# Performance work log

Hardware: AMD Instinct MI355X
Metric: run time of the kernel (lower is better)

The kernel has to match this reference:

```python
import jax, jax.numpy as jnp
import numpy as np

D = 1024; H = 16; DH = 64; L = 24; S = 4096; DFF = 4096
QB = 7; NC = 2 ** QB; TOPK = 10; EOS = NC + 1
SCALE = float(1.0 / np.sqrt(DH))


def _ln(x, g):
    m = jnp.mean(x, axis=-1, keepdims=True)
    v = jnp.var(x, axis=-1, keepdims=True)
    return (x - m) * jax.lax.rsqrt(v + 1e-5) * g


def _mlp(h, w1, b1, w2, b2, w3, b3):
    h = jax.nn.relu(h @ w1 + b1)
    h = jax.nn.relu(h @ w2 + b2)
    return h @ w3 + b3


def _decode(x, k_cache, v_cache, ln1_g, Wq, Wk, Wv, Wo, ln2_g, Wg, Wu, Wd, lnf_g):
    # single-token decode through L pre-norm layers with KV cache
    def step(h, xs):
        l1, wq, wk, wv, wo, l2, wg, wu, wd, K, V = xs
        hn = _ln(h, l1)
        q = (hn @ wq).reshape(H, DH)
        kn = (hn @ wk).reshape(1, H, DH)
        vn = (hn @ wv).reshape(1, H, DH)
        Kf = jnp.concatenate([K, kn], axis=0)  # [S+1,H,DH]
        Vf = jnp.concatenate([V, vn], axis=0)
        att = jax.nn.softmax(jnp.einsum('hd,shd->hs', q, Kf) * SCALE, axis=-1)
        o = jnp.einsum('hs,shd->hd', att, Vf).reshape(D)
        h = h + o @ wo
        hn = _ln(h, l2)
        h = h + (jax.nn.gelu(hn @ wg) * (hn @ wu)) @ wd  # GLU FF
        return h, None

    res, _ = jax.lax.scan(step, x, (ln1_g, Wq, Wk, Wv, Wo, ln2_g, Wg, Wu, Wd, k_cache, v_cache))
    return _ln(res, lnf_g)


def setup_inputs() -> dict:
    key = jax.random.key(0)
    ks = jax.random.split(key, 40)
    def r(i, shape, s=0.02):
        return jax.random.normal(ks[i], shape, dtype=jnp.float32) * s
    inp = {
        'x': r(0, (D,), 1.0),
        'k_cache': r(1, (L, S, H, DH), 1.0),
        'v_cache': r(2, (L, S, H, DH), 1.0),
        'ln1_g': jnp.ones((L, D), jnp.float32),
        'Wq': r(3, (L, D, D)), 'Wk': r(4, (L, D, D)), 'Wv': r(5, (L, D, D)), 'Wo': r(6, (L, D, D)),
        'ln2_g': jnp.ones((L, D), jnp.float32),
        'Wg': r(7, (L, D, DFF)), 'Wu': r(8, (L, D, DFF)), 'Wd': r(9, (L, DFF, D)),
        'lnf_g': jnp.ones((D,), jnp.float32),
        'h1_w1': r(10, (D, D)), 'h1_b1': jnp.zeros((D,), jnp.float32),
        'h1_w2': r(11, (D, D)), 'h1_b2': jnp.zeros((D,), jnp.float32),
        'h1_w3': r(12, (D, NC + 2)), 'h1_b3': jnp.zeros((NC + 2,), jnp.float32),
        'h2_w1': r(13, (2 * D, D)), 'h2_b1': jnp.zeros((D,), jnp.float32),
        'h2_w2': r(14, (D, D)), 'h2_b2': jnp.zeros((D,), jnp.float32),
        'h2_w3': r(15, (D, NC)), 'h2_b3': jnp.zeros((NC,), jnp.float32),
        'h3_w1': r(16, (3 * D, D)), 'h3_b1': jnp.zeros((D,), jnp.float32),
        'h3_w2': r(17, (D, D)), 'h3_b2': jnp.zeros((D,), jnp.float32),
        'h3_w3': r(18, (D, NC)), 'h3_b3': jnp.zeros((NC,), jnp.float32),
        'c1_emb': r(19, (NC, D), 1.0),
        'c2_emb': r(20, (NC, D), 1.0),
    }
    return inp


def reference(x, k_cache, v_cache, ln1_g, Wq, Wk, Wv, Wo, ln2_g, Wg, Wu, Wd, lnf_g,
              h1_w1, h1_b1, h1_w2, h1_b2, h1_w3, h1_b3,
              h2_w1, h2_b1, h2_w2, h2_b2, h2_w3, h2_b3,
              h3_w1, h3_b1, h3_w2, h3_b2, h3_w3, h3_b3,
              c1_emb, c2_emb):
    res = _decode(x, k_cache, v_cache, ln1_g, Wq, Wk, Wv, Wo, ln2_g, Wg, Wu, Wd, lnf_g)

    k1, k2, k3 = jax.random.split(jax.random.key(42), 3)

    # stage 1: z coordinate (quantized) with EOS-masked top-k sampling
    logits_z = _mlp(res, h1_w1, h1_b1, h1_w2, h1_b2, h1_w3, h1_b3)  # [NC+2]
    tpz, tiz = jax.lax.top_k(jax.nn.softmax(logits_z), TOPK)
    is_eos = tiz[0] == EOS
    mp = tpz * (tiz != EOS).astype(tpz.dtype)
    mp = mp / mp.sum()
    z = jnp.where(is_eos, EOS, tiz[jax.random.categorical(k1, jnp.log(mp + 1e-9))])
    emb_z = c1_emb[jnp.minimum(z, NC - 1)]

    # stage 2: y coordinate
    logits_y = _mlp(jnp.concatenate([res, emb_z]), h2_w1, h2_b1, h2_w2, h2_b2, h2_w3, h2_b3)
    tpy, tiy = jax.lax.top_k(jax.nn.softmax(logits_y), TOPK)
    y = tiy[jax.random.categorical(k2, jnp.log(tpy + 1e-9))]
    emb_y = c2_emb[y]

    # stage 3: x coordinate
    logits_x = _mlp(jnp.concatenate([res, emb_z, emb_y]), h3_w1, h3_b1, h3_w2, h3_b2, h3_w3, h3_b3)
    tpx, tix = jax.lax.top_k(jax.nn.softmax(logits_x), TOPK)
    xc = tix[jax.random.categorical(k3, jnp.log(tpx + 1e-9))]

    xyz = jnp.stack([xc, y, z])
    logits_cat = jnp.concatenate([logits_z, logits_y, logits_x])  # [130+128+128]=386
    return xyz, logits_cat
```

## Files before the change

kernel.cpp:

```cpp
#include <hip/hip_runtime.h>
#include <cstdint>
#include <cstring>
#include <cmath>

constexpr int kH    = 16;
constexpr int kL    = 24;
constexpr int kS    = 4096;
constexpr int kEOS  = 129;
constexpr float kSCALE = 0.125f;
constexpr int kNS   = 32;
constexpr int kTOK  = kS / kNS;

struct G10 { float g[10]; };


__device__ __forceinline__ float wave_sum(float v) {
  v += __shfl_xor(v, 32, 64); v += __shfl_xor(v, 16, 64);
  v += __shfl_xor(v, 8, 64);  v += __shfl_xor(v, 4, 64);
  v += __shfl_xor(v, 2, 64);  v += __shfl_xor(v, 1, 64);
  return v;
}
__device__ __forceinline__ float wave_max(float v) {
  v = fmaxf(v, __shfl_xor(v, 32, 64)); v = fmaxf(v, __shfl_xor(v, 16, 64));
  v = fmaxf(v, __shfl_xor(v, 8, 64));  v = fmaxf(v, __shfl_xor(v, 4, 64));
  v = fmaxf(v, __shfl_xor(v, 2, 64));  v = fmaxf(v, __shfl_xor(v, 1, 64));
  return v;
}
__device__ __forceinline__ float block_sum4(float v, float* red) {
  v = wave_sum(v);
  if ((threadIdx.x & 63) == 0) red[threadIdx.x >> 6] = v;
  __syncthreads();
  float s = red[0] + red[1] + red[2] + red[3];
  __syncthreads();
  return s;
}
__device__ __forceinline__ float block_max4(float v, float* red) {
  v = wave_max(v);
  if ((threadIdx.x & 63) == 0) red[threadIdx.x >> 6] = v;
  __syncthreads();
  float s = fmaxf(fmaxf(red[0], red[1]), fmaxf(red[2], red[3]));
  __syncthreads();
  return s;
}

__device__ __forceinline__ void ln_stats(const float* __restrict__ h, float* red,
                                         float& mean, float& rs) {
  int tid = threadIdx.x;
  float v0 = h[tid], v1 = h[tid + 256], v2 = h[tid + 512], v3 = h[tid + 768];
  float s = block_sum4(v0 + v1 + v2 + v3, red);
  mean = s * (1.0f / 1024.0f);
  float d0 = v0 - mean, d1 = v1 - mean, d2 = v2 - mean, d3 = v3 - mean;
  float sq = block_sum4(d0 * d0 + d1 * d1 + d2 * d2 + d3 * d3, red);
  rs = 1.0f / sqrtf(sq * (1.0f / 1024.0f) + 1e-5f);
}

__device__ __forceinline__ float gelu_f(float x) {
  float t = tanhf(0.7978845608028654f * (x + 0.044715f * x * x * x));
  return 0.5f * x * (1.0f + t);
}


__global__ __launch_bounds__(256) void k_ln_qkv(const float* __restrict__ h,
                                                const float* __restrict__ g,
                                                const float* __restrict__ Wq,
                                                const float* __restrict__ Wk,
                                                const float* __restrict__ Wv,
                                                float* __restrict__ qkv_part,
                                                float* __restrict__ hres) {
  __shared__ float red4[4];
  __shared__ float xs[64];
  __shared__ float4 sh4[256];
  int tid = threadIdx.x;
  float mean, rs;
  ln_stats(h, red4, mean, rs);
  int by = blockIdx.y, rb = by * 64;
  if (tid < 64) xs[tid] = (h[rb + tid] - mean) * rs * g[rb + tid];
  if (blockIdx.x == 0 && tid < 64) hres[rb + tid] = h[rb + tid];
  __syncthreads();
  int c4 = tid & 63, w = tid >> 6;
  int vcol4 = blockIdx.x * 64 + c4;
  int mat = vcol4 >> 8;
  const float* W = (mat == 0) ? Wq : ((mat == 1) ? Wk : Wv);
  const float4* W4 = reinterpret_cast<const float4*>(W);
  int wcol4 = vcol4 & 255;
  float4 acc = {0.f, 0.f, 0.f, 0.f};
  int r0 = w * 16;
  #pragma unroll
  for (int i = 0; i < 16; ++i) {
    int j = r0 + i;
    float xv = xs[j];
    float4 wv = W4[(size_t)(rb + j) * 256 + wcol4];
    acc.x += xv * wv.x; acc.y += xv * wv.y; acc.z += xv * wv.z; acc.w += xv * wv.w;
  }
  sh4[tid] = acc;
  __syncthreads();
  if (tid < 64) {
    float4 a = sh4[tid], b = sh4[tid + 64], c = sh4[tid + 128], d = sh4[tid + 192];
    a.x += b.x + c.x + d.x; a.y += b.y + c.y + d.y;
    a.z += b.z + c.z + d.z; a.w += b.w + c.w + d.w;
    reinterpret_cast<float4*>(qkv_part)[(size_t)by * 768 + blockIdx.x * 64 + tid] = a;
  }
}

__global__ __launch_bounds__(256) void k_attn(const float* __restrict__ qkv_part,
                                              const float* __restrict__ Kc,
                                              const float* __restrict__ Vc,
                                              float* __restrict__ part) {
  __shared__ float4 q4[16];
  __shared__ float4 kn4[16];
  __shared__ float4 vn4[16];
  __shared__ float sc[132];
  __shared__ float red4[4];
  __shared__ float4 ored[16][17];
  int split = blockIdx.x, head = blockIdx.y;
  int tid = threadIdx.x;
  if (tid < 64) {
    float s = 0.f;
    #pragma unroll
    for (int p = 0; p < 16; ++p) s += qkv_part[p * 3072 + head * 64 + tid];
    ((float*)q4)[tid] = s;
  } else if (tid < 128) {
    int d = tid - 64; float s = 0.f;
    #pragma unroll
    for (int p = 0; p < 16; ++p) s += qkv_part[p * 3072 + 1024 + head * 64 + d];
    ((float*)kn4)[d] = s;
  } else if (tid < 192) {
    int d = tid - 128; float s = 0.f;
    #pragma unroll
    for (int p = 0; p < 16; ++p) s += qkv_part[p * 3072 + 2048 + head * 64 + d];
    ((float*)vn4)[d] = s;
  }
  __syncthreads();
  int base = split * kTOK;
  int count = kTOK + (split == kNS - 1 ? 1 : 0);
  int wv = tid >> 6, lane = tid & 63, grp = lane >> 4, l16 = lane & 15;
  float4 qf = q4[l16];
  for (int t = wv * 4 + grp; t < count; t += 16) {
    float4 kf = (t < kTOK)
      ? reinterpret_cast<const float4*>(Kc + (size_t)(base + t) * 1024 + head * 64)[l16]
      : kn4[l16];
    float d = qf.x * kf.x + qf.y * kf.y + qf.z * kf.z + qf.w * kf.w;
    d += __shfl_xor(d, 1, 16); d += __shfl_xor(d, 2, 16);
    d += __shfl_xor(d, 4, 16); d += __shfl_xor(d, 8, 16);
    if (l16 == 0) sc[t] = d * kSCALE;
  }
  __syncthreads();
  float v = (tid < count) ? sc[tid] : -1e30f;
  float m = block_max4(v, red4);
  float pexp = 0.f;
  if (tid < count) { pexp = expf(sc[tid] - m); sc[tid] = pexp; }
  float l = block_sum4(pexp, red4);
  float4 acc = {0.f, 0.f, 0.f, 0.f};
  for (int t = wv * 4 + grp; t < count; t += 16) {
    float4 vf = (t < kTOK)
      ? reinterpret_cast<const float4*>(Vc + (size_t)(base + t) * 1024 + head * 64)[l16]
      : vn4[l16];
    float p = sc[t];
    acc.x += p * vf.x; acc.y += p * vf.y; acc.z += p * vf.z; acc.w += p * vf.w;
  }
  ored[wv * 4 + grp][l16] = acc;
  __syncthreads();
  float* pp = &part[(size_t)(head * kNS + split) * 68];
  if (tid < 16) {
    float4 s = ored[0][tid];
    #pragma unroll
    for (int k = 1; k < 16; ++k) {
      float4 b = ored[k][tid];
      s.x += b.x; s.y += b.y; s.z += b.z; s.w += b.w;
    }
    reinterpret_cast<float4*>(pp + 4)[tid] = s;
  }
  if (tid == 0) { pp[0] = m; pp[1] = l; }
}

__global__ __launch_bounds__(256) void k_comb_wo(const float* __restrict__ part,
                                                 const float* __restrict__ Wo,
                                                 float* __restrict__ hout) {
  __shared__ float o[64];
  __shared__ float4 sh4[256];
  int tid = threadIdx.x;
  int head = blockIdx.y;
  if (tid < 64) {
    const float* pp = part + (size_t)(head * kNS) * 68;
    float m = -1e30f;
    for (int s = 0; s < kNS; ++s) m = fmaxf(m, pp[s * 68]);
    float l = 0.f, acc = 0.f;
    for (int s = 0; s < kNS; ++s) {
      float e = expf(pp[s * 68] - m);
      l += e * pp[s * 68 + 1];
      acc += e * pp[s * 68 + 4 + tid];
    }
    o[tid] = acc / l;
  }
  __syncthreads();
  int c4 = tid & 63, w = tid >> 6;
  int vcol4 = blockIdx.x * 64 + c4;
  const float4* W4 = reinterpret_cast<const float4*>(Wo);
  float4 acc = {0.f, 0.f, 0.f, 0.f};
  int r0 = w * 16;
  #pragma unroll
  for (int i = 0; i < 16; ++i) {
    int r = r0 + i;
    float xv = o[r];
    float4 wv = W4[(size_t)(head * 64 + r) * 256 + vcol4];
    acc.x += xv * wv.x; acc.y += xv * wv.y; acc.z += xv * wv.z; acc.w += xv * wv.w;
  }
  sh4[tid] = acc;
  __syncthreads();
  if (tid < 64) {
    float4 a = sh4[tid], b = sh4[tid + 64], c = sh4[tid + 128], d = sh4[tid + 192];
    a.x += b.x + c.x + d.x; a.y += b.y + c.y + d.y;
    a.z += b.z + c.z + d.z; a.w += b.w + c.w + d.w;
    int vcol = (blockIdx.x * 64 + tid) * 4;
    atomicAdd(&hout[vcol],     a.x);
    atomicAdd(&hout[vcol + 1], a.y);
    atomicAdd(&hout[vcol + 2], a.z);
    atomicAdd(&hout[vcol + 3], a.w);
  }
}

__global__ __launch_bounds__(256) void k_ln_gu(const float* __restrict__ h,
                                               const float* __restrict__ g,
                                               const float* __restrict__ Wg,
                                               const float* __restrict__ Wu,
                                               float* __restrict__ gu_part,
                                               float* __restrict__ hres) {
  __shared__ float red4[4];
  __shared__ float xs[64];
  __shared__ float4 sh4[256];
  int tid = threadIdx.x;
  float mean, rs;
  ln_stats(h, red4, mean, rs);
  int by = blockIdx.y, rb = by * 64;
  if (tid < 64) xs[tid] = (h[rb + tid] - mean) * rs * g[rb + tid];
  if (blockIdx.x == 0 && tid < 64) hres[rb + tid] = h[rb + tid];
  __syncthreads();
  int c4 = tid & 63, w = tid >> 6;
  int vcol4 = blockIdx.x * 64 + c4;
  int mat = vcol4 >> 10;
  const float4* W4 = reinterpret_cast<const float4*>(mat ? Wu : Wg);
  int wcol4 = vcol4 & 1023;
  float4 acc = {0.f, 0.f, 0.f, 0.f};
  int r0 = w * 16;
  #pragma unroll
  for (int i = 0; i < 16; ++i) {
    int j = r0 + i;
    float xv = xs[j];
    float4 wv = W4[(size_t)(rb + j) * 1024 + wcol4];
    acc.x += xv * wv.x; acc.y += xv * wv.y; acc.z += xv * wv.z; acc.w += xv * wv.w;
  }
  sh4[tid] = acc;
  __syncthreads();
  if (tid < 64) {
    float4 a = sh4[tid], b = sh4[tid + 64], c = sh4[tid + 128], d = sh4[tid + 192];
    a.x += b.x + c.x + d.x; a.y += b.y + c.y + d.y;
    a.z += b.z + c.z + d.z; a.w += b.w + c.w + d.w;
    reinterpret_cast<float4*>(gu_part)[(size_t)by * 2048 + blockIdx.x * 64 + tid] = a;
  }
}

__global__ __launch_bounds__(256) void k_act_wd(const float* __restrict__ gu_part,
                                                const float* __restrict__ Wd,
                                                float* __restrict__ hout) {
  __shared__ float xs[64];
  __shared__ float4 sh4[256];
  int tid = threadIdx.x;
  int by = blockIdx.y, rb = by * 64;
  if (tid < 64) {
    float gs = 0.f, us = 0.f;
    #pragma unroll
    for (int p = 0; p < 16; ++p) {
      gs += gu_part[p * 8192 + rb + tid];
      us += gu_part[p * 8192 + 4096 + rb + tid];
    }
    xs[tid] = gelu_f(gs) * us;
  }
  __syncthreads();
  int c4 = tid & 63, w = tid >> 6;
  int vcol4 = blockIdx.x * 64 + c4;
  const float4* W4 = reinterpret_cast<const float4*>(Wd);
  float4 acc = {0.f, 0.f, 0.f, 0.f};
  int r0 = w * 16;
  #pragma unroll
  for (int i = 0; i < 16; ++i) {
    int j = r0 + i;
    float xv = xs[j];
    float4 wv = W4[(size_t)(rb + j) * 256 + vcol4];
    acc.x += xv * wv.x; acc.y += xv * wv.y; acc.z += xv * wv.z; acc.w += xv * wv.w;
  }
  sh4[tid] = acc;
  __syncthreads();
  if (tid < 64) {
    float4 a = sh4[tid], b = sh4[tid + 64], c = sh4[tid + 128], d = sh4[tid + 192];
    a.x += b.x + c.x + d.x; a.y += b.y + c.y + d.y;
    a.z += b.z + c.z + d.z; a.w += b.w + c.w + d.w;
    int vcol = (blockIdx.x * 64 + tid) * 4;
    atomicAdd(&hout[vcol],     a.x);
    atomicAdd(&hout[vcol + 1], a.y);
    atomicAdd(&hout[vcol + 2], a.z);
    atomicAdd(&hout[vcol + 3], a.w);
  }
}


__global__ __launch_bounds__(256) void k_lnf(const float* __restrict__ h,
                                             const float* __restrict__ g,
                                             float* __restrict__ outv) {
  __shared__ float red4[4];
  int tid = threadIdx.x;
  float mean, rs;
  ln_stats(h, red4, mean, rs);
  #pragma unroll
  for (int k = 0; k < 4; ++k) {
    int i = tid + 256 * k;
    outv[i] = (h[i] - mean) * rs * g[i];
  }
}

__global__ __launch_bounds__(256) void k_head_g1(const float* __restrict__ x,
                                                 const float* __restrict__ W,
                                                 float* __restrict__ t1_part,
                                                 const float* __restrict__ b3,
                                                 float* __restrict__ logits, int n3) {
  __shared__ float4 sh4[256];
  int tid = threadIdx.x;
  int by = blockIdx.y, rb = by * 64;
  if (blockIdx.x == 0 && by == 0 && tid < n3) logits[tid] = b3[tid];
  int c4 = tid & 63, w = tid >> 6;
  int vcol4 = blockIdx.x * 64 + c4;
  const float4* W4 = reinterpret_cast<const float4*>(W);
  float4 acc = {0.f, 0.f, 0.f, 0.f};
  int r0 = w * 16;
  #pragma unroll
  for (int i = 0; i < 16; ++i) {
    int r = rb + r0 + i;
    float xv = x[r];
    float4 wv = W4[(size_t)r * 256 + vcol4];
    acc.x += xv * wv.x; acc.y += xv * wv.y; acc.z += xv * wv.z; acc.w += xv * wv.w;
  }
  sh4[tid] = acc;
  __syncthreads();
  if (tid < 64) {
    float4 a = sh4[tid], b = sh4[tid + 64], c = sh4[tid + 128], d = sh4[tid + 192];
    a.x += b.x + c.x + d.x; a.y += b.y + c.y + d.y;
    a.z += b.z + c.z + d.z; a.w += b.w + c.w + d.w;
    reinterpret_cast<float4*>(t1_part)[(size_t)by * 256 + blockIdx.x * 64 + tid] = a;
  }
}

__global__ __launch_bounds__(256) void k_head_g2(const float* __restrict__ t1_part,
                                                 int ny,
                                                 const float* __restrict__ b1,
                                                 const float* __restrict__ W,
                                                 float* __restrict__ t2_part) {
  __shared__ float xs[64];
  __shared__ float4 sh4[256];
  int tid = threadIdx.x;
  int by = blockIdx.y, rb = by * 64;
  if (tid < 64) {
    float s = b1[rb + tid];
    for (int p = 0; p < ny; ++p) s += t1_part[p * 1024 + rb + tid];
    xs[tid] = fmaxf(s, 0.f);
  }
  __syncthreads();
  int c4 = tid & 63, w = tid >> 6;
  int vcol4 = blockIdx.x * 64 + c4;
  const float4* W4 = reinterpret_cast<const float4*>(W);
  float4 acc = {0.f, 0.f, 0.f, 0.f};
  int r0 = w * 16;
  #pragma unroll
  for (int i = 0; i < 16; ++i) {
    int j = r0 + i;
    float xv = xs[j];
    float4 wv = W4[(size_t)(rb + j) * 256 + vcol4];
    acc.x += xv * wv.x; acc.y += xv * wv.y; acc.z += xv * wv.z; acc.w += xv * wv.w;
  }
  sh4[tid] = acc;
  __syncthreads();
  if (tid < 64) {
    float4 a = sh4[tid], b = sh4[tid + 64], c = sh4[tid + 128], d = sh4[tid + 192];
    a.x += b.x + c.x + d.x; a.y += b.y + c.y + d.y;
    a.z += b.z + c.z + d.z; a.w += b.w + c.w + d.w;
    reinterpret_cast<float4*>(t2_part)[(size_t)by * 256 + blockIdx.x * 64 + tid] = a;
  }
}

__global__ __launch_bounds__(256) void k_head_g3(const float* __restrict__ t2_part,
                                                 const float* __restrict__ b2,
                                                 const float* __restrict__ W,
                                                 float* __restrict__ logits, int n3) {
  __shared__ float xs[64];
  int tid = threadIdx.x;
  int rb = blockIdx.x * 64;
  if (tid < 64) {
    float s = b2[rb + tid];
    #pragma unroll
    for (int p = 0; p < 16; ++p) s += t2_part[p * 1024 + rb + tid];
    xs[tid] = fmaxf(s, 0.f);
  }
  __syncthreads();
  if (tid < n3) {
    float acc = 0.f;
    for (int i = 0; i < 64; ++i) acc += xs[i] * W[(size_t)(rb + i) * n3 + tid];
    atomicAdd(&logits[tid], acc);
  }
}


__global__ void k_sample1(const float* __restrict__ logits,
                          const float* __restrict__ c1_emb,
                          float* __restrict__ embdst,
                          float* __restrict__ out_xyz,
                          G10 gb) {
  __shared__ int zsh;
  int tid = threadIdx.x;
  if (tid == 0) {
    float p[130];
    float mx = -1e30f;
    for (int i = 0; i < 130; ++i) mx = fmaxf(mx, logits[i]);
    float s = 0.f;
    for (int i = 0; i < 130; ++i) { p[i] = expf(logits[i] - mx); s += p[i]; }
    for (int i = 0; i < 130; ++i) p[i] /= s;
    float tp[10]; int ti[10];
    for (int k = 0; k < 10; ++k) {
      float best = -1.f; int bi = 0;
      for (int i = 0; i < 130; ++i)
        if (p[i] > best) { best = p[i]; bi = i; }
      tp[k] = best; ti[k] = bi; p[bi] = -2.f;
    }
    int is_eos = (ti[0] == kEOS);
    float mp[10]; float ssum = 0.f;
    for (int k = 0; k < 10; ++k) {
      mp[k] = tp[k] * ((ti[k] != kEOS) ? 1.f : 0.f);
      ssum += mp[k];
    }
    float bestsc = -1e30f; int ba = 0;
    for (int k = 0; k < 10; ++k) {
      float sc = logf(mp[k] / ssum + 1e-9f) + gb.g[k];
      if (sc > bestsc) { bestsc = sc; ba = k; }
    }
    int z = is_eos ? kEOS : ti[ba];
    zsh = z;
    out_xyz[2] = (float)z;
  }
  __syncthreads();
  int zi = zsh; if (zi > 127) zi = 127;
  for (int i = tid; i < 1024; i += blockDim.x)
    embdst[i] = c1_emb[(size_t)zi * 1024 + i];
}

__global__ void k_sample23(const float* __restrict__ logits,
                           const float* __restrict__ emb,
                           float* __restrict__ embdst,
                           float* __restrict__ outslot,
                           G10 gb) {
  __shared__ int ysh;
  int tid = threadIdx.x;
  if (tid == 0) {
    float p[128];
    float mx = -1e30f;
    for (int i = 0; i < 128; ++i) mx = fmaxf(mx, logits[i]);
    float s = 0.f;
    for (int i = 0; i < 128; ++i) { p[i] = expf(logits[i] - mx); s += p[i]; }
    for (int i = 0; i < 128; ++i) p[i] /= s;
    float tp[10]; int ti[10];
    for (int k = 0; k < 10; ++k) {
      float best = -1.f; int bi = 0;
      for (int i = 0; i < 128; ++i)
        if (p[i] > best) { best = p[i]; bi = i; }
      tp[k] = best; ti[k] = bi; p[bi] = -2.f;
    }
    float bestsc = -1e30f; int ba = 0;
    for (int k = 0; k < 10; ++k) {
      float sc = logf(tp[k] + 1e-9f) + gb.g[k];
      if (sc > bestsc) { bestsc = sc; ba = k; }
    }
    int y = ti[ba];
    ysh = y;
    *outslot = (float)y;
  }
  __syncthreads();
  if (emb != nullptr) {
    int y = ysh;
    for (int i = tid; i < 1024; i += blockDim.x)
      embdst[i] = emb[(size_t)y * 1024 + i];
  }
}


static inline uint32_t rotl32(uint32_t x, uint32_t r) { return (x << r) | (x >> (32 - r)); }

static void threefry2x32(uint32_t k0, uint32_t k1, uint32_t x0, uint32_t x1,
                         uint32_t* o0, uint32_t* o1) {
  uint32_t ks0 = k0, ks1 = k1, ks2 = k0 ^ k1 ^ 0x1BD11BDAu;
  const uint32_t R0[4] = {13, 15, 26, 6};
  const uint32_t R1[4] = {17, 29, 16, 24};
  x0 += ks0; x1 += ks1;
  for (int j = 0; j < 4; ++j) { x0 += x1; x1 = rotl32(x1, R0[j]); x1 ^= x0; }
  x0 += ks1; x1 += ks2 + 1u;
  for (int j = 0; j < 4; ++j) { x0 += x1; x1 = rotl32(x1, R1[j]); x1 ^= x0; }
  x0 += ks2; x1 += ks0 + 2u;
  for (int j = 0; j < 4; ++j) { x0 += x1; x1 = rotl32(x1, R0[j]); x1 ^= x0; }
  x0 += ks0; x1 += ks1 + 3u;
  for (int j = 0; j < 4; ++j) { x0 += x1; x1 = rotl32(x1, R1[j]); x1 ^= x0; }
  x0 += ks1; x1 += ks2 + 4u;
  for (int j = 0; j < 4; ++j) { x0 += x1; x1 = rotl32(x1, R0[j]); x1 ^= x0; }
  x0 += ks2; x1 += ks0 + 5u;
  *o0 = x0; *o1 = x1;
}

static void gumbel10_part(uint32_t k0, uint32_t k1, float* g) {
  const float tiny = 1.1754943508222875e-38f;
  for (int i = 0; i < 10; ++i) {
    uint32_t a, c;
    threefry2x32(k0, k1, 0u, (uint32_t)i, &a, &c);
    uint32_t bits = a ^ c;
    uint32_t fb = (bits >> 9) | 0x3f800000u;
    float f; memcpy(&f, &fb, 4);
    f -= 1.0f;
    float u = f * (1.0f - tiny) + tiny;
    if (u < tiny) u = tiny;
    g[i] = -logf(-logf(u));
  }
}


extern "C" void kernel_launch(void* const* d_in, const int* in_sizes, int n_in,
                              void* d_out, int out_size, void* d_ws, size_t ws_size,
                              hipStream_t stream) {
  (void)in_sizes; (void)n_in; (void)out_size; (void)ws_size;
  const float* x      = (const float*)d_in[0];
  const float* kcache = (const float*)d_in[1];
  const float* vcache = (const float*)d_in[2];
  const float* ln1g   = (const float*)d_in[3];
  const float* Wq     = (const float*)d_in[4];
  const float* Wk     = (const float*)d_in[5];
  const float* Wv     = (const float*)d_in[6];
  const float* Wo     = (const float*)d_in[7];
  const float* ln2g   = (const float*)d_in[8];
  const float* Wg     = (const float*)d_in[9];
  const float* Wu     = (const float*)d_in[10];
  const float* Wd     = (const float*)d_in[11];
  const float* lnfg   = (const float*)d_in[12];
  const float* h1w1 = (const float*)d_in[13]; const float* h1b1 = (const float*)d_in[14];
  const float* h1w2 = (const float*)d_in[15]; const float* h1b2 = (const float*)d_in[16];
  const float* h1w3 = (const float*)d_in[17]; const float* h1b3 = (const float*)d_in[18];
  const float* h2w1 = (const float*)d_in[19]; const float* h2b1 = (const float*)d_in[20];
  const float* h2w2 = (const float*)d_in[21]; const float* h2b2 = (const float*)d_in[22];
  const float* h2w3 = (const float*)d_in[23]; const float* h2b3 = (const float*)d_in[24];
  const float* h3w1 = (const float*)d_in[25]; const float* h3b1 = (const float*)d_in[26];
  const float* h3w2 = (const float*)d_in[27]; const float* h3b2 = (const float*)d_in[28];
  const float* h3w3 = (const float*)d_in[29]; const float* h3b3 = (const float*)d_in[30];
  const float* c1emb = (const float*)d_in[31];
  const float* c2emb = (const float*)d_in[32];

  float* ws = (float*)d_ws;
  float* hA   = ws;
  float* hB   = ws + 1024;
  float* qkvp = ws + 2048;
  float* part = ws + 51200;
  float* gup  = ws + 86016;
  float* cat  = ws + 217088;
  float* t1p  = gup;
  float* t2p  = gup + 49152;
  float* out  = (float*)d_out;

  hipMemcpyAsync(hA, x, 1024 * sizeof(float), hipMemcpyDeviceToDevice, stream);

  for (int l = 0; l < kL; ++l) {
    const float* Wq_l = Wq + (size_t)l * 1024 * 1024;
    const float* Wk_l = Wk + (size_t)l * 1024 * 1024;
    const float* Wv_l = Wv + (size_t)l * 1024 * 1024;
    const float* Wo_l = Wo + (size_t)l * 1024 * 1024;
    const float* Wg_l = Wg + (size_t)l * 1024 * 4096;
    const float* Wu_l = Wu + (size_t)l * 1024 * 4096;
    const float* Wd_l = Wd + (size_t)l * 4096 * 1024;
    const float* Kc_l = kcache + (size_t)l * kS * 1024;
    const float* Vc_l = vcache + (size_t)l * kS * 1024;

    k_ln_qkv<<<dim3(12, 16), 256, 0, stream>>>(hA, ln1g + (size_t)l * 1024,
                                               Wq_l, Wk_l, Wv_l, qkvp, hB);
    k_attn<<<dim3(kNS, kH), 256, 0, stream>>>(qkvp, Kc_l, Vc_l, part);
    k_comb_wo<<<dim3(4, kH), 256, 0, stream>>>(part, Wo_l, hB);
    k_ln_gu<<<dim3(32, 16), 256, 0, stream>>>(hB, ln2g + (size_t)l * 1024,
                                              Wg_l, Wu_l, gup, hA);
    k_act_wd<<<dim3(4, 64), 256, 0, stream>>>(gup, Wd_l, hA);
  }

  k_lnf<<<1, 256, 0, stream>>>(hA, lnfg, cat);

  uint32_t k1a, k1b, k2a, k2b, k3a, k3b;
  threefry2x32(0u, 42u, 0u, 0u, &k1a, &k1b);
  threefry2x32(0u, 42u, 0u, 1u, &k2a, &k2b);
  threefry2x32(0u, 42u, 0u, 2u, &k3a, &k3b);
  G10 G1, G2, G3;
  gumbel10_part(k1a, k1b, G1.g);
  gumbel10_part(k2a, k2b, G2.g);
  gumbel10_part(k3a, k3b, G3.g);

  k_head_g1<<<dim3(4, 16), 256, 0, stream>>>(cat, h1w1, t1p, h1b3, out + 3, 130);
  k_head_g2<<<dim3(4, 16), 256, 0, stream>>>(t1p, 16, h1b1, h1w2, t2p);
  k_head_g3<<<16, 256, 0, stream>>>(t2p, h1b2, h1w3, out + 3, 130);
  k_sample1<<<1, 256, 0, stream>>>(out + 3, c1emb, cat + 1024, out, G1);

  k_head_g1<<<dim3(4, 32), 256, 0, stream>>>(cat, h2w1, t1p, h2b3, out + 133, 128);
  k_head_g2<<<dim3(4, 16), 256, 0, stream>>>(t1p, 32, h2b1, h2w2, t2p);
  k_head_g3<<<16, 256, 0, stream>>>(t2p, h2b2, h2w3, out + 133, 128);
  k_sample23<<<1, 256, 0, stream>>>(out + 133, c2emb, cat + 2048, out + 1, G2);

  k_head_g1<<<dim3(4, 48), 256, 0, stream>>>(cat, h3w1, t1p, h3b3, out + 261, 128);
  k_head_g2<<<dim3(4, 16), 256, 0, stream>>>(t1p, 48, h3b1, h3w2, t2p);
  k_head_g3<<<16, 256, 0, stream>>>(t2p, h3b2, h3w3, out + 261, 128);
  k_sample23<<<1, 256, 0, stream>>>(out + 261, nullptr, nullptr, out + 0, G3);
}
```

Measured before the change: 1.361 ms.

## Fuse attention with Wo and GLU with Wd using atomic-counter last-block handoff

Merges the attention split kernel with the combine+Wo projection, and the LN+gate/up kernel with the activation+Wd projection, into two cooperative kernels. Per-head and per-slice atomic counters let the last-arriving blocks spin-wait for their peers and then do the dependent reduction and matvec, which removes two launches per layer (48 in total). The cost is spin-waiting blocks, extra fences and atomics, and reliance on cooperative launch to guarantee co-residency. The Wd stage is also remapped to 16-row chunks per block, with atomics to hA per thread.

```diff
diff --git a/kernel.cpp b/kernel.cpp
--- a/kernel.cpp
+++ b/kernel.cpp
@@ -102,16 +102,22 @@
   }
 }
 
-__global__ __launch_bounds__(256) void k_attn(const float* __restrict__ qkv_part,
-                                              const float* __restrict__ Kc,
-                                              const float* __restrict__ Vc,
-                                              float* __restrict__ part) {
+__global__ __launch_bounds__(256, 2) void k_attn_wo(const float* __restrict__ qkv_part,
+                                                    const float* __restrict__ Kc,
+                                                    const float* __restrict__ Vc,
+                                                    float* __restrict__ part,
+                                                    const float* __restrict__ Wo,
+                                                    float* __restrict__ hB,
+                                                    unsigned* __restrict__ cnt,
+                                                    unsigned base) {
   __shared__ float4 q4[16];
   __shared__ float4 kn4[16];
   __shared__ float4 vn4[16];
   __shared__ float sc[132];
   __shared__ float red4[4];
   __shared__ float4 ored[16][17];
+  __shared__ float osh[64];
+  __shared__ unsigned oldsh;
   int split = blockIdx.x, head = blockIdx.y;
   int tid = threadIdx.x;
   if (tid < 64) {
@@ -131,13 +137,13 @@
     ((float*)vn4)[d] = s;
   }
   __syncthreads();
-  int base = split * kTOK;
+  int basetok = split * kTOK;
   int count = kTOK + (split == kNS - 1 ? 1 : 0);
   int wv = tid >> 6, lane = tid & 63, grp = lane >> 4, l16 = lane & 15;
   float4 qf = q4[l16];
   for (int t = wv * 4 + grp; t < count; t += 16) {
     float4 kf = (t < kTOK)
-      ? reinterpret_cast<const float4*>(Kc + (size_t)(base + t) * 1024 + head * 64)[l16]
+      ? reinterpret_cast<const float4*>(Kc + (size_t)(basetok + t) * 1024 + head * 64)[l16]
       : kn4[l16];
     float d = qf.x * kf.x + qf.y * kf.y + qf.z * kf.z + qf.w * kf.w;
     d += __shfl_xor(d, 1, 16); d += __shfl_xor(d, 2, 16);
@@ -149,14 +155,14 @@
   float m = block_max4(v, red4);
   float pexp = 0.f;
   if (tid < count) { pexp = expf(sc[tid] - m); sc[tid] = pexp; }
-  float l = block_sum4(pexp, red4);
+  float lsum = block_sum4(pexp, red4);
   float4 acc = {0.f, 0.f, 0.f, 0.f};
   for (int t = wv * 4 + grp; t < count; t += 16) {
     float4 vf = (t < kTOK)
-      ? reinterpret_cast<const float4*>(Vc + (size_t)(base + t) * 1024 + head * 64)[l16]
+      ? reinterpret_cast<const float4*>(Vc + (size_t)(basetok + t) * 1024 + head * 64)[l16]
       : vn4[l16];
-    float p = sc[t];
-    acc.x += p * vf.x; acc.y += p * vf.y; acc.z += p * vf.z; acc.w += p * vf.w;
+    float pw = sc[t];
+    acc.x += pw * vf.x; acc.y += pw * vf.y; acc.z += pw * vf.z; acc.w += pw * vf.w;
   }
   ored[wv * 4 + grp][l16] = acc;
   __syncthreads();
@@ -170,73 +176,90 @@
     }
     reinterpret_cast<float4*>(pp + 4)[tid] = s;
   }
-  if (tid == 0) { pp[0] = m; pp[1] = l; }
-}
-
-__global__ __launch_bounds__(256) void k_comb_wo(const float* __restrict__ part,
-                                                 const float* __restrict__ Wo,
-                                                 float* __restrict__ hout) {
-  __shared__ float o[64];
-  __shared__ float4 sh4[256];
-  int tid = threadIdx.x;
-  int head = blockIdx.y;
-  if (tid < 64) {
-    const float* pp = part + (size_t)(head * kNS) * 68;
-    float m = -1e30f;
-    for (int s = 0; s < kNS; ++s) m = fmaxf(m, pp[s * 68]);
-    float l = 0.f, acc = 0.f;
+  if (tid == 0) { pp[0] = m; pp[1] = lsum; }
+  __syncthreads();
+
+  if (tid == 0) {
+    __threadfence();
+    oldsh = __hip_atomic_fetch_add(&cnt[head * 32], 1u, __ATOMIC_ACQ_REL,
+                                   __HIP_MEMORY_SCOPE_AGENT);
+  }
+  __syncthreads();
+  unsigned old = oldsh;
+  if (old < base + 28u) return;
+  int colblk = (int)(old - base - 28u);
+  if (tid == 0) {
+    while (__hip_atomic_load(&cnt[head * 32], __ATOMIC_ACQUIRE,
+                             __HIP_MEMORY_SCOPE_AGENT) < base + 32u)
+      __builtin_amdgcn_s_sleep(4);
+  }
+  __syncthreads();
+  __threadfence();
+
+  if (tid < 64) {
+    const float* ph = part + (size_t)(head * kNS) * 68;
+    float mm = -1e30f;
+    for (int s = 0; s < kNS; ++s) mm = fmaxf(mm, ph[s * 68]);
+    float ll = 0.f, ac = 0.f;
     for (int s = 0; s < kNS; ++s) {
-      float e = expf(pp[s * 68] - m);
-      l += e * pp[s * 68 + 1];
-      acc += e * pp[s * 68 + 4 + tid];
-    }
-    o[tid] = acc / l;
-  }
-  __syncthreads();
-  int c4 = tid & 63, w = tid >> 6;
-  int vcol4 = blockIdx.x * 64 + c4;
+      float e = expf(ph[s * 68] - mm);
+      ll += e * ph[s * 68 + 1];
+      ac += e * ph[s * 68 + 4 + tid];
+    }
+    osh[tid] = ac / ll;
+  }
+  __syncthreads();
+  float4* shw = &ored[0][0];
+  int c4 = tid & 63, w2 = tid >> 6;
+  int vcol4 = colblk * 64 + c4;
   const float4* W4 = reinterpret_cast<const float4*>(Wo);
-  float4 acc = {0.f, 0.f, 0.f, 0.f};
-  int r0 = w * 16;
+  float4 ac2 = {0.f, 0.f, 0.f, 0.f};
+  int r0 = w2 * 16;
   #pragma unroll
   for (int i = 0; i < 16; ++i) {
     int r = r0 + i;
-    float xv = o[r];
+    float xv = osh[r];
     float4 wv = W4[(size_t)(head * 64 + r) * 256 + vcol4];
-    acc.x += xv * wv.x; acc.y += xv * wv.y; acc.z += xv * wv.z; acc.w += xv * wv.w;
-  }
-  sh4[tid] = acc;
-  __syncthreads();
-  if (tid < 64) {
-    float4 a = sh4[tid], b = sh4[tid + 64], c = sh4[tid + 128], d = sh4[tid + 192];
+    ac2.x += xv * wv.x; ac2.y += xv * wv.y; ac2.z += xv * wv.z; ac2.w += xv * wv.w;
+  }
+  shw[tid] = ac2;
+  __syncthreads();
+  if (tid < 64) {
+    float4 a = shw[tid], b = shw[tid + 64], c = shw[tid + 128], d = shw[tid + 192];
     a.x += b.x + c.x + d.x; a.y += b.y + c.y + d.y;
     a.z += b.z + c.z + d.z; a.w += b.w + c.w + d.w;
-    int vcol = (blockIdx.x * 64 + tid) * 4;
-    atomicAdd(&hout[vcol],     a.x);
-    atomicAdd(&hout[vcol + 1], a.y);
-    atomicAdd(&hout[vcol + 2], a.z);
-    atomicAdd(&hout[vcol + 3], a.w);
-  }
-}
-
-__global__ __launch_bounds__(256) void k_ln_gu(const float* __restrict__ h,
-                                               const float* __restrict__ g,
-                                               const float* __restrict__ Wg,
-                                               const float* __restrict__ Wu,
-                                               float* __restrict__ gu_part,
-                                               float* __restrict__ hres) {
+    int vcol = (colblk * 64 + tid) * 4;
+    atomicAdd(&hB[vcol],     a.x);
+    atomicAdd(&hB[vcol + 1], a.y);
+    atomicAdd(&hB[vcol + 2], a.z);
+    atomicAdd(&hB[vcol + 3], a.w);
+  }
+}
+
+__global__ __launch_bounds__(256, 2) void k_gu_wd(const float* __restrict__ hB,
+                                                  const float* __restrict__ g,
+                                                  const float* __restrict__ Wg,
+                                                  const float* __restrict__ Wu,
+                                                  float* __restrict__ gup,
+                                                  float* __restrict__ hA,
+                                                  const float* __restrict__ Wd,
+                                                  unsigned* __restrict__ cntS,
+                                                  unsigned* __restrict__ cntCP,
+                                                  unsigned baseS, unsigned baseCP) {
   __shared__ float red4[4];
   __shared__ float xs[64];
   __shared__ float4 sh4[256];
-  int tid = threadIdx.x;
+  __shared__ unsigned oldsh;
+  int tid = threadIdx.x;
+  int bx = blockIdx.x, by = blockIdx.y;
   float mean, rs;
-  ln_stats(h, red4, mean, rs);
-  int by = blockIdx.y, rb = by * 64;
-  if (tid < 64) xs[tid] = (h[rb + tid] - mean) * rs * g[rb + tid];
-  if (blockIdx.x == 0 && tid < 64) hres[rb + tid] = h[rb + tid];
+  ln_stats(hB, red4, mean, rs);
+  int rb = by * 64;
+  if (tid < 64) xs[tid] = (hB[rb + tid] - mean) * rs * g[rb + tid];
+  if (bx == 0 && tid < 64) hA[rb + tid] = hB[rb + tid];
   __syncthreads();
   int c4 = tid & 63, w = tid >> 6;
-  int vcol4 = blockIdx.x * 64 + c4;
+  int vcol4 = bx * 64 + c4;
   int mat = vcol4 >> 10;
   const float4* W4 = reinterpret_cast<const float4*>(mat ? Wu : Wg);
   int wcol4 = vcol4 & 1023;
@@ -255,51 +278,59 @@
     float4 a = sh4[tid], b = sh4[tid + 64], c = sh4[tid + 128], d = sh4[tid + 192];
     a.x += b.x + c.x + d.x; a.y += b.y + c.y + d.y;
     a.z += b.z + c.z + d.z; a.w += b.w + c.w + d.w;
-    reinterpret_cast<float4*>(gu_part)[(size_t)by * 2048 + blockIdx.x * 64 + tid] = a;
-  }
-}
-
-__global__ __launch_bounds__(256) void k_act_wd(const float* __restrict__ gu_part,
-                                                const float* __restrict__ Wd,
-                                                float* __restrict__ hout) {
-  __shared__ float xs[64];
-  __shared__ float4 sh4[256];
-  int tid = threadIdx.x;
-  int by = blockIdx.y, rb = by * 64;
-  if (tid < 64) {
+    reinterpret_cast<float4*>(gup)[(size_t)by * 2048 + bx * 64 + tid] = a;
+  }
+  __syncthreads();
+
+  int s = bx & 15;
+  if (tid == 0) {
+    __threadfence();
+    if (bx == 0)
+      __hip_atomic_fetch_add(&cntCP[0], 1u, __ATOMIC_ACQ_REL, __HIP_MEMORY_SCOPE_AGENT);
+    oldsh = __hip_atomic_fetch_add(&cntS[s * 32], 1u, __ATOMIC_ACQ_REL,
+                                   __HIP_MEMORY_SCOPE_AGENT);
+  }
+  __syncthreads();
+  unsigned old = oldsh;
+  if (old < baseS + 16u) return;
+  int chunk16 = (int)(old - baseS - 16u);
+  if (tid == 0) {
+    while (__hip_atomic_load(&cntS[s * 32], __ATOMIC_ACQUIRE,
+                             __HIP_MEMORY_SCOPE_AGENT) < baseS + 32u ||
+           __hip_atomic_load(&cntCP[0], __ATOMIC_ACQUIRE,
+                             __HIP_MEMORY_SCOPE_AGENT) < baseCP + 16u)
+      __builtin_amdgcn_s_sleep(4);
+  }
+  __syncthreads();
+  __threadfence();
+
+  int rowbase = s * 256 + chunk16 * 16;
+  float* gt  = (float*)sh4;
+  float* ut  = ((float*)sh4) + 256;
+  float* act = ((float*)sh4) + 512;
+  int q = tid >> 4, r = tid & 15;
+  gt[tid] = gup[q * 8192 + rowbase + r];
+  ut[tid] = gup[q * 8192 + 4096 + rowbase + r];
+  __syncthreads();
+  if (tid < 16) {
     float gs = 0.f, us = 0.f;
     #pragma unroll
-    for (int p = 0; p < 16; ++p) {
-      gs += gu_part[p * 8192 + rb + tid];
-      us += gu_part[p * 8192 + 4096 + rb + tid];
-    }
-    xs[tid] = gelu_f(gs) * us;
-  }
-  __syncthreads();
-  int c4 = tid & 63, w = tid >> 6;
-  int vcol4 = blockIdx.x * 64 + c4;
-  const float4* W4 = reinterpret_cast<const float4*>(Wd);
-  float4 acc = {0.f, 0.f, 0.f, 0.f};
-  int r0 = w * 16;
+    for (int qq = 0; qq < 16; ++qq) { gs += gt[qq * 16 + tid]; us += ut[qq * 16 + tid]; }
+    act[tid] = gelu_f(gs) * us;
+  }
+  __syncthreads();
+  const float4* Wd4 = reinterpret_cast<const float4*>(Wd);
+  float4 a2 = {0.f, 0.f, 0.f, 0.f};
   #pragma unroll
   for (int i = 0; i < 16; ++i) {
-    int j = r0 + i;
-    float xv = xs[j];
-    float4 wv = W4[(size_t)(rb + j) * 256 + vcol4];
-    acc.x += xv * wv.x; acc.y += xv * wv.y; acc.z += xv * wv.z; acc.w += xv * wv.w;
-  }
-  sh4[tid] = acc;
-  __syncthreads();
-  if (tid < 64) {
-    float4 a = sh4[tid], b = sh4[tid + 64], c = sh4[tid + 128], d = sh4[tid + 192];
-    a.x += b.x + c.x + d.x; a.y += b.y + c.y + d.y;
-    a.z += b.z + c.z + d.z; a.w += b.w + c.w + d.w;
-    int vcol = (blockIdx.x * 64 + tid) * 4;
-    atomicAdd(&hout[vcol],     a.x);
-    atomicAdd(&hout[vcol + 1], a.y);
-    atomicAdd(&hout[vcol + 2], a.z);
-    atomicAdd(&hout[vcol + 3], a.w);
-  }
+    float xv = act[i];
+    float4 wv = Wd4[(size_t)(rowbase + i) * 256 + tid];
+    a2.x += xv * wv.x; a2.y += xv * wv.y; a2.z += xv * wv.z; a2.w += xv * wv.w;
+  }
+  atomicAdd(&hA[tid * 4],     a2.x);
+  atomicAdd(&hA[tid * 4 + 1], a2.y);
+  atomicAdd(&hA[tid * 4 + 2], a2.z);
+  atomicAdd(&hA[tid * 4 + 3], a2.w);
 }
 
 
@@ -561,10 +592,16 @@
   float* part = ws + 51200;
   float* gup  = ws + 86016;
   float* cat  = ws + 217088;
+  float* t2p  = ws + 220160;
+  unsigned* bar = (unsigned*)(ws + 236544);
   float* t1p  = gup;
-  float* t2p  = gup + 49152;
   float* out  = (float*)d_out;
 
+  unsigned* cntH  = bar;
+  unsigned* cntS  = bar + 512;
+  unsigned* cntCP = bar + 1024;
+
+  hipMemsetAsync(bar, 0, 1056 * sizeof(unsigned), stream);
   hipMemcpyAsync(hA, x, 1024 * sizeof(float), hipMemcpyDeviceToDevice, stream);
 
   for (int l = 0; l < kL; ++l) {
@@ -577,14 +614,30 @@
     const float* Wd_l = Wd + (size_t)l * 4096 * 1024;
     const float* Kc_l = kcache + (size_t)l * kS * 1024;
     const float* Vc_l = vcache + (size_t)l * kS * 1024;
-
-    k_ln_qkv<<<dim3(12, 16), 256, 0, stream>>>(hA, ln1g + (size_t)l * 1024,
-                                               Wq_l, Wk_l, Wv_l, qkvp, hB);
-    k_attn<<<dim3(kNS, kH), 256, 0, stream>>>(qkvp, Kc_l, Vc_l, part);
-    k_comb_wo<<<dim3(4, kH), 256, 0, stream>>>(part, Wo_l, hB);
-    k_ln_gu<<<dim3(32, 16), 256, 0, stream>>>(hB, ln2g + (size_t)l * 1024,
-                                              Wg_l, Wu_l, gup, hA);
-    k_act_wd<<<dim3(4, 64), 256, 0, stream>>>(gup, Wd_l, hA);
+    const float* ln1_l = ln1g + (size_t)l * 1024;
+    const float* ln2_l = ln2g + (size_t)l * 1024;
+
+    k_ln_qkv<<<dim3(12, 16), 256, 0, stream>>>(hA, ln1_l, Wq_l, Wk_l, Wv_l, qkvp, hB);
+
+    {
+      unsigned base = (unsigned)l * 32u;
+      const float* a0 = qkvp; const float* a1 = Kc_l; const float* a2 = Vc_l;
+      float* a3 = part; const float* a4 = Wo_l; float* a5 = hB;
+      unsigned* a6 = cntH; unsigned a7 = base;
+      void* args[] = {&a0, &a1, &a2, &a3, &a4, &a5, &a6, &a7};
+      hipLaunchCooperativeKernel((void*)k_attn_wo, dim3(kNS, kH), dim3(256), args, 0, stream);
+    }
+
+    {
+      unsigned baseS = (unsigned)l * 32u, baseCP = (unsigned)l * 16u;
+      const float* a0 = hB; const float* a1 = ln2_l;
+      const float* a2 = Wg_l; const float* a3 = Wu_l;
+      float* a4 = gup; float* a5 = hA; const float* a6 = Wd_l;
+      unsigned* a7 = cntS; unsigned* a8 = cntCP;
+      unsigned a9 = baseS, a10 = baseCP;
+      void* args[] = {&a0, &a1, &a2, &a3, &a4, &a5, &a6, &a7, &a8, &a9, &a10};
+      hipLaunchCooperativeKernel((void*)k_gu_wd, dim3(32, 16), dim3(256), args, 0, stream);
+    }
   }
 
   k_lnf<<<1, 256, 0, stream>>>(hA, lnfg, cat);
```

New measurement: 4.751 ms. 249% more time.
